# Optimization experiments

Measured on AMD Instinct MI355X. Metric: run time of the kernel, lower is better.

## Reference

```python
import jax, jax.numpy as jnp
import numpy as np
from jax import lax

B, T, CIN, H, W = 2, 6, 1, 256, 256
COUT = 64
L = 13
H2, W2 = H // 2, W // 2


def conv2d(x, w, b, stride=1, pad=0):
    y = lax.conv_general_dilated(x, w, (stride, stride), [(pad, pad), (pad, pad)],
                                 dimension_numbers=('NCHW', 'OIHW', 'NCHW'))
    return y + b[None, :, None, None]


def leaky(x):
    return jnp.where(x >= 0, x, 0.2 * x)


def bilinear_sample(img, sx, sy):
    # img [B,C,H,W]; sx,sy [B,L,H,W] pixel coords; zero padding (grid_sample align_corners=True)
    Bc, C, Hh, Ww = img.shape
    x0 = jnp.floor(sx); y0 = jnp.floor(sy)
    x1 = x0 + 1.0; y1 = y0 + 1.0
    wx1 = sx - x0; wx0 = 1.0 - wx1
    wy1 = sy - y0; wy0 = 1.0 - wy1
    img_flat = img.reshape(Bc, C, Hh * Ww)

    def gather(xi, yi):
        valid = (xi >= 0) & (xi <= Ww - 1) & (yi >= 0) & (yi <= Hh - 1)
        xc = jnp.clip(xi, 0, Ww - 1).astype(jnp.int32)
        yc = jnp.clip(yi, 0, Hh - 1).astype(jnp.int32)
        idx = (yc * Ww + xc).reshape(Bc, 1, -1)
        g = jnp.take_along_axis(img_flat, idx, axis=2).reshape(Bc, C, *xi.shape[1:])
        return g * valid[:, None].astype(img.dtype)  # [B,C,L,H,W]

    return (gather(x0, y0) * (wx0 * wy0)[:, None]
            + gather(x1, y0) * (wx1 * wy0)[:, None]
            + gather(x0, y1) * (wx0 * wy1)[:, None]
            + gather(x1, y1) * (wx1 * wy1)[:, None])


def setup_inputs() -> dict:
    key = jax.random.key(0)
    ks = jax.random.split(key, 14)
    s = 0.05
    return {
        'x': jax.random.normal(ks[0], (B, T, CIN, H, W), jnp.float32),
        'w_stem': jax.random.normal(ks[1], (COUT * T, CIN * T, 3, 3), jnp.float32) * s,
        'b_stem': jnp.zeros((COUT * T,), jnp.float32),
        'w_i2h': jax.random.normal(ks[2], (3 * COUT, COUT, 3, 3), jnp.float32) * s,
        'b_i2h': jnp.zeros((3 * COUT,), jnp.float32),
        'w_i2f': jax.random.normal(ks[3], (32, COUT, 5, 5), jnp.float32) * s,
        'b_i2f': jnp.zeros((32,), jnp.float32),
        'w_h2f': jax.random.normal(ks[4], (32, COUT, 5, 5), jnp.float32) * s,
        'b_h2f': jnp.zeros((32,), jnp.float32),
        'w_flow': jax.random.normal(ks[5], (L * 2, 32, 5, 5), jnp.float32) * s,
        'b_flow': jnp.zeros((L * 2,), jnp.float32),
        'w_ret': jax.random.normal(ks[6], (3 * COUT, L * COUT, 1, 1), jnp.float32) * s,
        'b_ret': jnp.zeros((3 * COUT,), jnp.float32),
    }


def reference(x, w_stem, b_stem, w_i2h, b_i2h, w_i2f, b_i2f, w_h2f, b_h2f,
              w_flow, b_flow, w_ret, b_ret):
    Bq, Tq, Cq, Hq, Wq = x.shape
    h2, w2 = Hq // 2, Wq // 2
    # stem: fold T into channels, strided conv + leaky relu
    xs = x.reshape(Bq, Tq * Cq, Hq, Wq)
    ys = leaky(conv2d(xs, w_stem, b_stem, stride=2, pad=1))
    ys = ys.reshape(Bq, Tq, COUT, h2, w2)
    seq = jnp.transpose(ys, (1, 0, 2, 3, 4))  # [T,B,C,h,w]

    gy, gx = jnp.meshgrid(jnp.arange(h2, dtype=jnp.float32),
                          jnp.arange(w2, dtype=jnp.float32), indexing='ij')

    def step(hprev, xt):
        i2h = conv2d(xt, w_i2h, b_i2h, pad=1)  # [B,3C,h,w]
        f1 = leaky(conv2d(xt, w_i2f, b_i2f, pad=2) + conv2d(hprev, w_h2f, b_h2f, pad=2))
        flows = conv2d(f1, w_flow, b_flow, pad=2).reshape(Bq, L, 2, h2, w2)
        u, v = flows[:, :, 0], flows[:, :, 1]
        # wrap(h, -flow): sample at grid - flow
        sx = gx[None, None] - u
        sy = gy[None, None] - v
        warped = bilinear_sample(hprev, sx, sy)  # [B,C,L,h,w]
        warped = jnp.transpose(warped, (0, 2, 1, 3, 4)).reshape(Bq, L * COUT, h2, w2)
        h2h = conv2d(warped, w_ret, b_ret)  # 1x1 conv
        ir, iu, im = jnp.split(i2h, 3, axis=1)
        hr, hu, hm = jnp.split(h2h, 3, axis=1)
        r = jax.nn.sigmoid(ir + hr)
        z = jax.nn.sigmoid(iu + hu)
        m = leaky(im + r * hm)
        hnext = z * hprev + (1.0 - z) * m
        return hnext, hnext

    h0 = jnp.zeros((Bq, COUT, h2, w2), x.dtype)
    _, outs = lax.scan(step, h0, seq)  # [T,B,C,h,w]
    return jnp.transpose(outs, (1, 0, 2, 3, 4))
```

## Files before the change

kernel.cpp:

```cpp
#include <hip/hip_runtime.h>
#include <cstddef>

#define NPIX 16384
#define T_ 6

typedef __attribute__((ext_vector_type(8))) short bf16x8;
typedef __attribute__((ext_vector_type(4))) short bf16x4;
typedef __attribute__((ext_vector_type(4))) float f32x4;
typedef __attribute__((ext_vector_type(4))) unsigned u32x4;
typedef __attribute__((ext_vector_type(2))) unsigned u32x2;

__device__ __forceinline__ float leakyf(float x){ return x >= 0.f ? x : 0.2f*x; }
__device__ __forceinline__ float sigmf(float x){ return 1.f/(1.f+__expf(-x)); }
__device__ __forceinline__ short f2bf(float f){
    unsigned u = __float_as_uint(f);
    u += 0x7fffu + ((u>>16)&1u);
    return (short)(u>>16);
}
__device__ __forceinline__ float bf2f(short s){
    return __uint_as_float(((unsigned)(unsigned short)s)<<16);
}
__device__ __forceinline__ unsigned cvtpk(float lo, float hi){
    unsigned d;
    asm("v_cvt_pk_bf16_f32 %0, %1, %2" : "=v"(d) : "v"(lo), "v"(hi));
    return d;
}
__device__ __forceinline__ f32x4 MFMA(bf16x8 a, bf16x8 b, f32x4 c){
    return __builtin_amdgcn_mfma_f32_16x16x32_bf16(a, b, c, 0, 0, 0);
}

__global__ __launch_bounds__(256) void prep_w(const float* __restrict__ wi2h,
        const float* __restrict__ wf1i, const float* __restrict__ wf1h,
        const float* __restrict__ wfl, const float* __restrict__ wrt,
        const float* __restrict__ wst, short* __restrict__ dst){
    int idx = blockIdx.x*256 + threadIdx.x;
    float v;
    if(idx < 110592){
        int kk = idx/12288, r = idx%12288, oc = r>>6, ic = r&63;
        v = wi2h[((size_t)(oc*64+ic))*9 + kk];
    } else if(idx < 212992){
        int j = idx-110592; int tap = j>>11, r = j&2047, oc = r>>6, ic = r&63;
        int inp = tap/25, q = tap%25;
        const float* s = inp ? wf1h : wf1i;
        v = s[((size_t)(oc*64+ic))*25 + q];
    } else if(idx < 238592){
        int j = idx-212992; int q = j>>10, r = j&1023, oc = r>>5, ic = r&31;
        v = (oc < 26) ? wfl[((size_t)(oc*32+ic))*25 + q] : 0.f;
    } else if(idx < 398336){
        int j = idx-238592; int s_ = j/6144, r = j%6144, oc = r>>5, c = r&31;
        v = wrt[(size_t)oc*832 + s_*32 + c];
    } else {
        int j = idx-398336; int oc = j>>6, k = j&63;
        if(k < 54){ int ic = k/9, kk = k%9; v = wst[((size_t)(oc*6+ic))*9 + kk]; }
        else v = 0.f;
    }
    dst[idx] = f2bf(v);
}

__global__ __launch_bounds__(256) void stem_mfma(const float* __restrict__ x,
        const short* __restrict__ wS, const float* __restrict__ bias, short* __restrict__ ys_cl){
    __shared__ float xh[6*17*18];
    int bx = blockIdx.x;
    int ohalf = bx & 1, tile = (bx>>1) & 255, b = bx>>9;
    int ty0 = (tile>>4)*8, tx0 = (tile&15)*8;
    int tid = threadIdx.x, wid = tid>>6, lane = tid&63, lr = lane&15, lg = lane>>4;
    int iy0 = ty0*2-1, ix0 = tx0*2-1;
    for(int i=tid; i<1734; i+=256){
        int ic = i/289, r = i%289, hy = r/17, hx = r%17;
        int iy = iy0+hy, ix = ix0+hx;
        float v = 0.f;
        if((unsigned)iy<256u && (unsigned)ix<256u) v = x[((size_t)b*6+ic)*65536 + iy*256 + ix];
        xh[(ic*17+hy)*18+hx] = v;
    }
    __syncthreads();
    int pxl = wid*16 + lr;
    int ry = (pxl>>3)*2, rx = (pxl&7)*2;
    bf16x8 a[2];
    #pragma unroll
    for(int cg=0; cg<2; ++cg){
        #pragma unroll
        for(int e=0; e<8; ++e){
            int k = cg*32 + lg*8 + e;
            float v = 0.f;
            if(k < 54){
                int ic = k/9, t9 = k%9, ky = t9/3, kx = t9%3;
                v = xh[(ic*17 + ry+ky)*18 + rx+kx];
            }
            a[cg][e] = f2bf(v);
        }
    }
    short* yb = ys_cl + (size_t)b*NPIX*384;
    #pragma unroll
    for(int nj=0; nj<12; ++nj){
        int oc = (ohalf*12 + nj)*16 + lr;
        f32x4 acc = {};
        #pragma unroll
        for(int cg=0; cg<2; ++cg){
            bf16x8 bb = *(const bf16x8*)&wS[(size_t)oc*64 + cg*32 + lg*8];
            acc = MFMA(a[cg], bb, acc);
        }
        float bvs = bias[oc];
        #pragma unroll
        for(int r=0; r<4; ++r){
            int pxr = wid*16 + lg*4 + r;
            int pix = (ty0 + (pxr>>3))*128 + tx0 + (pxr&7);
            yb[(size_t)pix*384 + oc] = f2bf(leakyf(acc[r]+bvs));
        }
    }
}

__global__ __launch_bounds__(512) void ih_if_mfma(const short* __restrict__ ys_cl,
        const short* __restrict__ wI, const float* __restrict__ bI,
        const short* __restrict__ wF,
        short* __restrict__ i2h_all, float* __restrict__ f1i_all){
    __shared__ short xt[432*72];
    int bx = blockIdx.x;
    int tile = bx & 63; int r_ = bx >> 6; int t = r_ % 6; int b = r_ / 6;
    int ty0 = (tile>>2)*8, tx0 = (tile&3)*32;
    int tid = threadIdx.x, wid = tid>>6, lane = tid&63, lr = lane&15, lg = lane>>4;
    int mw = wid>>2, nw = wid&3;
    const short* xb = ys_cl + (size_t)b*NPIX*384 + t*64;
    for(int i=tid; i<3456; i+=512){
        int pix = i>>3, c8 = i&7;
        int hy = pix/36, hx = pix - hy*36;
        int py = ty0 - 2 + hy, px = tx0 - 2 + hx;
        bf16x8 v = {};
        if((unsigned)py < 128u && (unsigned)px < 128u)
            v = *(const bf16x8*)&xb[((size_t)py*128 + px)*384 + c8*8];
        *(bf16x8*)&xt[pix*72 + c8*8] = v;
    }
    __syncthreads();
    f32x4 accI[4][2][3] = {};
    for(int kk=0; kk<9; ++kk){
        int ky = kk/3, kx = kk - ky*3;
        #pragma unroll
        for(int cg=0; cg<2; ++cg){
            bf16x8 bv[3];
            #pragma unroll
            for(int ni=0; ni<3; ++ni)
                bv[ni] = *(const bf16x8*)&wI[((size_t)kk*192 + nw*48 + ni*16 + lr)*64 + cg*32 + lg*8];
            #pragma unroll
            for(int ri=0; ri<4; ++ri){
                int r2 = mw*4 + ri;
                bf16x8 av[2];
                #pragma unroll
                for(int mi=0; mi<2; ++mi){
                    int hp = (r2 + ky + 1)*36 + mi*16 + lr + kx + 1;
                    av[mi] = *(const bf16x8*)&xt[hp*72 + cg*32 + lg*8];
                }
                #pragma unroll
                for(int mi=0; mi<2; ++mi)
                  #pragma unroll
                  for(int ni=0; ni<3; ++ni)
                    accI[ri][mi][ni] = MFMA(av[mi], bv[ni], accI[ri][mi][ni]);
            }
        }
    }
    short* oI = i2h_all + ((size_t)t*2 + b)*192*NPIX;
    #pragma unroll
    for(int ri=0; ri<4; ++ri){
        int py = ty0 + mw*4 + ri;
        #pragma unroll
        for(int mi=0; mi<2; ++mi){
            int px = tx0 + mi*16 + lg*4;
            #pragma unroll
            for(int ni=0; ni<3; ++ni){
                int oc = nw*48 + ni*16 + lr;
                float bvs = bI[oc];
                f32x4 r = accI[ri][mi][ni];
                u32x2 st;
                st[0] = cvtpk(r[0]+bvs, r[1]+bvs);
                st[1] = cvtpk(r[2]+bvs, r[3]+bvs);
                *(u32x2*)&oI[(size_t)oc*NPIX + py*128 + px] = st;
            }
        }
    }
    f32x4 accF[4] = {};
    int mif = nw>>1, jF = (nw&1)*16 + lr;
    for(int q=0; q<25; ++q){
        int ky = q/5, kx = q - ky*5;
        #pragma unroll
        for(int cg=0; cg<2; ++cg){
            bf16x8 bb = *(const bf16x8*)&wF[((size_t)q*32 + (nw&1)*16 + lr)*64 + cg*32 + lg*8];
            #pragma unroll
            for(int ri=0; ri<4; ++ri){
                int hp = (mw*4 + ri + ky)*36 + mif*16 + lr + kx;
                bf16x8 av = *(const bf16x8*)&xt[hp*72 + cg*32 + lg*8];
                accF[ri] = MFMA(av, bb, accF[ri]);
            }
        }
    }
    float* oF = f1i_all + ((size_t)t*2 + b)*32*NPIX;
    #pragma unroll
    for(int ri=0; ri<4; ++ri){
        int py = ty0 + mw*4 + ri;
        int px = tx0 + mif*16 + lg*4;
        *(f32x4*)&oF[(size_t)jF*NPIX + py*128 + px] = accF[ri];
    }
}

__global__ __launch_bounds__(256) void f1h_mfma(const short* __restrict__ h_cl,
        const short* __restrict__ wF, const float* __restrict__ f1i_all, int t,
        const float* __restrict__ bi, const float* __restrict__ bh,
        short* __restrict__ f1_cl){
    __shared__ short xt[144*72];
    int bx = blockIdx.x;
    int tile = bx & 255, b = bx>>8;
    int ty0 = (tile>>4)*8, tx0 = (tile&15)*8;
    int tid = threadIdx.x, wid = tid>>6, lane = tid&63, lr = lane&15, lg = lane>>4;
    int mw = wid>>1, nw = wid&1;
    const short* xb = h_cl + (size_t)b*NPIX*64;
    for(int i=tid; i<1152; i+=256){
        int pix = i>>3, c8 = i&7;
        int hy = pix/12, hx = pix - hy*12;
        int py = ty0 - 2 + hy, px = tx0 - 2 + hx;
        bf16x8 v = {};
        if((unsigned)py < 128u && (unsigned)px < 128u)
            v = *(const bf16x8*)&xb[((size_t)py*128 + px)*64 + c8*8];
        *(bf16x8*)&xt[pix*72 + c8*8] = v;
    }
    __syncthreads();
    f32x4 acc[2] = {};
    for(int q=0; q<25; ++q){
        int ky = q/5, kx = q - ky*5;
        #pragma unroll
        for(int cg=0; cg<2; ++cg){
            bf16x8 av[2];
            #pragma unroll
            for(int mi=0; mi<2; ++mi){
                int m = mw*32 + mi*16 + lr;
                int hp = ((m>>3)+ky)*12 + (m&7)+kx;
                av[mi] = *(const bf16x8*)&xt[hp*72 + cg*32 + lg*8];
            }
            bf16x8 bb = *(const bf16x8*)&wF[((size_t)(25+q)*32 + nw*16 + lr)*64 + cg*32 + lg*8];
            #pragma unroll
            for(int mi=0; mi<2; ++mi) acc[mi] = MFMA(av[mi], bb, acc[mi]);
        }
    }
    int j = nw*16 + lr;
    float bvs = bi[j] + bh[j];
    const float* pF = f1i_all + ((size_t)t*2 + b)*32*NPIX;
    __syncthreads();
    #pragma unroll
    for(int mi=0; mi<2; ++mi){
        int m0 = mw*32 + mi*16 + lg*4;
        int py = ty0 + (m0>>3), px = tx0 + (m0&7);
        f32x4 p = *(const f32x4*)&pF[(size_t)j*NPIX + py*128 + px];
        #pragma unroll
        for(int r=0; r<4; ++r) xt[(m0+r)*40 + j] = f2bf(leakyf(acc[mi][r] + p[r] + bvs));
    }
    __syncthreads();
    {
        int px = tid>>2, c8 = tid&3;
        int pix = (ty0 + (px>>3))*128 + tx0 + (px&7);
        *(bf16x8*)&f1_cl[((size_t)b*NPIX + pix)*32 + c8*8] = *(const bf16x8*)&xt[px*40 + c8*8];
    }
}

__global__ __launch_bounds__(256) void flow_mfma(const short* __restrict__ f1_cl,
        const short* __restrict__ wA, const float* __restrict__ bias, float* __restrict__ flows){
    __shared__ short xt[144*40];
    int bx = blockIdx.x;
    int tile = bx & 255, b = bx>>8;
    int ty0 = (tile>>4)*8, tx0 = (tile&15)*8;
    int tid = threadIdx.x, wid = tid>>6, lane = tid&63, lr = lane&15, lg = lane>>4;
    int mw = wid>>1, nw = wid&1;
    f32x4 acc[2] = {};
    const short* xb = f1_cl + (size_t)b*NPIX*32;
    for(int i=tid; i<576; i+=256){
        int pix = i>>2, c8 = i&3;
        int hy = pix/12, hx = pix - hy*12;
        int py = ty0 - 2 + hy, px = tx0 - 2 + hx;
        bf16x8 v = {};
        if((unsigned)py < 128u && (unsigned)px < 128u)
            v = *(const bf16x8*)&xb[((size_t)py*128 + px)*32 + c8*8];
        *(bf16x8*)&xt[pix*40 + c8*8] = v;
    }
    __syncthreads();
    for(int ky=0; ky<5; ++ky){
        #pragma unroll
        for(int kx=0; kx<5; ++kx){
            bf16x8 av[2];
            #pragma unroll
            for(int mi=0; mi<2; ++mi){
                int m = mw*32 + mi*16 + lr;
                int hp = ((m>>3)+ky)*12 + (m&7) + kx;
                av[mi] = *(const bf16x8*)&xt[hp*40 + lg*8];
            }
            bf16x8 bb = *(const bf16x8*)&wA[((size_t)((ky*5+kx)*32) + nw*16 + lr)*32 + lg*8];
            #pragma unroll
            for(int mi=0; mi<2; ++mi) acc[mi] = MFMA(av[mi], bb, acc[mi]);
        }
    }
    int j = nw*16 + lr;
    if(j < 26){
        float bvs = bias[j];
        #pragma unroll
        for(int mi=0; mi<2; ++mi){
            int m0 = mw*32 + mi*16 + lg*4;
            int py = ty0 + (m0>>3), px = tx0 + (m0&7);
            f32x4 r = acc[mi];
            f32x4 st; st[0]=r[0]+bvs; st[1]=r[1]+bvs; st[2]=r[2]+bvs; st[3]=r[3]+bvs;
            *(f32x4*)&flows[((size_t)b*26 + j)*NPIX + py*128 + px] = st;
        }
    }
}

__device__ __forceinline__ void calc_corners(const float* __restrict__ s_sx,
        const float* __restrict__ s_sy, int l, int mypx,
        int& i00, int& i10, int& i01, int& i11,
        float& w00, float& w10, float& w01, float& w11){
    float sx = s_sx[l*64+mypx], sy = s_sy[l*64+mypx];
    float x0f = floorf(sx), y0f = floorf(sy);
    int x0 = (int)x0f, y0 = (int)y0f;
    float wx1 = sx-x0f, wy1 = sy-y0f, wx0 = 1.f-wx1, wy0 = 1.f-wy1;
    bool vx0 = (unsigned)x0<128u, vx1 = (unsigned)(x0+1)<128u;
    bool vy0 = (unsigned)y0<128u, vy1 = (unsigned)(y0+1)<128u;
    w00 = (vx0&&vy0)? wx0*wy0 : 0.f;
    w10 = (vx1&&vy0)? wx1*wy0 : 0.f;
    w01 = (vx0&&vy1)? wx0*wy1 : 0.f;
    w11 = (vx1&&vy1)? wx1*wy1 : 0.f;
    int xc0 = max(0,min(127,x0)), xc1 = max(0,min(127,x0+1));
    int yc0 = max(0,min(127,y0)), yc1 = max(0,min(127,y0+1));
    i00 = yc0*128+xc0; i10 = yc0*128+xc1; i01 = yc1*128+xc0; i11 = yc1*128+xc1;
}

__global__ __launch_bounds__(256) void warpret_mfma(
        const float* __restrict__ hprev_f32, int hstride,
        const short* __restrict__ h_in,
        const float* __restrict__ flows,
        const short* __restrict__ wret, const float* __restrict__ b_ret,
        const short* __restrict__ ib_bf, float* __restrict__ out,
        short* __restrict__ h_out, int t){
    __shared__ float s_sx[832], s_sy[832];
    __shared__ short At[2][64*40];
    __shared__ short Bt[2][192*40];
    int bx = blockIdx.x;
    int half = bx & 1, row = (bx>>1) & 127, b = bx >> 8;
    int pxbase = half*64;
    int tid = threadIdx.x, wid = tid>>6, lane = tid&63, lr = lane&15, lg = lane>>4;
    const short* hc = h_in + (size_t)b*NPIX*64;
    f32x4 acc[12] = {};
    for(int i=tid; i<832; i+=256){
        int l = i>>6, px = i&63;
        float u = flows[((size_t)b*26 + 2*l)*NPIX + row*128 + pxbase + px];
        float v = flows[((size_t)b*26 + 2*l+1)*NPIX + row*128 + pxbase + px];
        s_sx[i] = (float)(pxbase+px) - u;
        s_sy[i] = (float)row - v;
    }
    __syncthreads();

    int spx = tid & 63, sch = tid >> 6;
    int brow = tid >> 2, bc4 = tid & 3;

    auto issue = [&](int sp, bf16x8& g00, bf16x8& g10, bf16x8& g01, bf16x8& g11,
                     bf16x8& q0, bf16x8& q1, bf16x8& q2,
                     float& w00, float& w10, float& w01, float& w11){
        int i00,i10,i01,i11;
        calc_corners(s_sx, s_sy, sp>>1, spx, i00,i10,i01,i11, w00,w10,w01,w11);
        int cb = (sp&1)*32 + sch*8;
        g00 = *(const bf16x8*)&hc[(size_t)i00*64 + cb];
        g10 = *(const bf16x8*)&hc[(size_t)i10*64 + cb];
        g01 = *(const bf16x8*)&hc[(size_t)i01*64 + cb];
        g11 = *(const bf16x8*)&hc[(size_t)i11*64 + cb];
        q0 = *(const bf16x8*)&wret[((size_t)sp*192 + brow      )*32 + bc4*8];
        q1 = *(const bf16x8*)&wret[((size_t)sp*192 + brow +  64)*32 + bc4*8];
        q2 = *(const bf16x8*)&wret[((size_t)sp*192 + brow + 128)*32 + bc4*8];
    };
    auto commit = [&](int buf, bf16x8 g00, bf16x8 g10, bf16x8 g01, bf16x8 g11,
                      bf16x8 q0, bf16x8 q1, bf16x8 q2,
                      float w00, float w10, float w01, float w11){
        float r[8];
        #pragma unroll
        for(int e=0; e<8; ++e)
            r[e] = bf2f(g00[e])*w00 + bf2f(g10[e])*w10 +
                   bf2f(g01[e])*w01 + bf2f(g11[e])*w11;
        u32x4 av;
        av[0] = cvtpk(r[0], r[1]);
        av[1] = cvtpk(r[2], r[3]);
        av[2] = cvtpk(r[4], r[5]);
        av[3] = cvtpk(r[6], r[7]);
        *(u32x4*)&At[buf][spx*40 + sch*8] = av;
        *(bf16x8*)&Bt[buf][(brow      )*40 + bc4*8] = q0;
        *(bf16x8*)&Bt[buf][(brow +  64)*40 + bc4*8] = q1;
        *(bf16x8*)&Bt[buf][(brow + 128)*40 + bc4*8] = q2;
    };

    {
        bf16x8 g00,g10,g01,g11,q0,q1,q2; float w00,w10,w01,w11;
        issue(0, g00,g10,g01,g11,q0,q1,q2, w00,w10,w01,w11);
        commit(0, g00,g10,g01,g11,q0,q1,q2, w00,w10,w01,w11);
    }
    bf16x8 p00,p10,p01,p11,pq0,pq1,pq2; float v00,v10,v01,v11;
    issue(1, p00,p10,p01,p11,pq0,pq1,pq2, v00,v10,v01,v11);
    __syncthreads();

    for(int s=0; s<26; ++s){
        int cur = s & 1, nxt = cur ^ 1;
        bf16x8 n00,n10,n01,n11,nq0,nq1,nq2; float u00,u10,u01,u11;
        if(s < 24)
            issue(s+2, n00,n10,n01,n11,nq0,nq1,nq2, u00,u10,u01,u11);
        {
            bf16x8 a = *(const bf16x8*)&At[cur][(wid*16 + lr)*40 + lg*8];
            #pragma unroll
            for(int ni=0; ni<12; ++ni){
                bf16x8 bb = *(const bf16x8*)&Bt[cur][(ni*16 + lr)*40 + lg*8];
                acc[ni] = MFMA(a, bb, acc[ni]);
            }
        }
        if(s < 25)
            commit(nxt, p00,p10,p01,p11,pq0,pq1,pq2, v00,v10,v01,v11);
        __syncthreads();
        if(s < 24){
            p00=n00; p10=n10; p01=n01; p11=n11;
            pq0=nq0; pq1=nq1; pq2=nq2;
            v00=u00; v10=u10; v01=u01; v11=u11;
        }
    }

    short* Ht = &Bt[0][0];
    const short* ib = ib_bf + (size_t)b*192*NPIX + row*128 + pxbase;
    const float* hbf = hprev_f32 + (size_t)b*hstride + row*128 + pxbase;
    float* ob = out + (((size_t)b*T_ + t)*64)*NPIX + row*128 + pxbase;
    int px4 = wid*16 + lg*4;
    #pragma unroll
    for(int ni=0; ni<4; ++ni){
        int oc = ni*16 + lr;
        bf16x4 irv = *(const bf16x4*)&ib[(size_t)oc*NPIX + px4];
        bf16x4 iuv = *(const bf16x4*)&ib[(size_t)(64+oc)*NPIX + px4];
        bf16x4 imv = *(const bf16x4*)&ib[(size_t)(128+oc)*NPIX + px4];
        f32x4 hp = *(const f32x4*)&hbf[(size_t)oc*NPIX + px4];
        float br = b_ret[oc], bu = b_ret[64+oc], bm = b_ret[128+oc];
        f32x4 st;
        #pragma unroll
        for(int r=0; r<4; ++r){
            float hr = acc[ni][r] + br;
            float hu = acc[ni+4][r] + bu;
            float hm = acc[ni+8][r] + bm;
            float rg = sigmf(bf2f(irv[r]) + hr);
            float zg = sigmf(bf2f(iuv[r]) + hu);
            float mg = leakyf(bf2f(imv[r]) + rg*hm);
            st[r] = zg*hp[r] + (1.f-zg)*mg;
        }
        *(f32x4*)&ob[(size_t)oc*NPIX + px4] = st;
        #pragma unroll
        for(int r=0; r<4; ++r) Ht[(px4+r)*72 + oc] = f2bf(st[r]);
    }
    __syncthreads();
    short* ho = h_out + ((size_t)b*NPIX + row*128 + pxbase)*64;
    for(int i=tid; i<512; i+=256){
        int px = i>>3, c8 = i&7;
        *(bf16x8*)&ho[(size_t)px*64 + c8*8] = *(const bf16x8*)&Ht[px*72 + c8*8];
    }
}

extern "C" void kernel_launch(void* const* d_in, const int* in_sizes, int n_in,
                              void* d_out, int out_size, void* d_ws, size_t ws_size,
                              hipStream_t stream) {
    const float* x      = (const float*)d_in[0];
    const float* w_stem = (const float*)d_in[1];
    const float* b_stem = (const float*)d_in[2];
    const float* w_i2h  = (const float*)d_in[3];
    const float* b_i2h  = (const float*)d_in[4];
    const float* w_i2f  = (const float*)d_in[5];
    const float* b_i2f  = (const float*)d_in[6];
    const float* w_h2f  = (const float*)d_in[7];
    const float* b_h2f  = (const float*)d_in[8];
    const float* w_flow = (const float*)d_in[9];
    const float* b_flow = (const float*)d_in[10];
    const float* w_ret  = (const float*)d_in[11];
    const float* b_ret  = (const float*)d_in[12];
    float* out = (float*)d_out;

    char* w = (char*)d_ws;
    float* h0_f32  = (float*)w;  w += (size_t)2*64*NPIX*4;
    short* i2h_all = (short*)w;  w += (size_t)6*2*192*NPIX*2;
    float* f1i_all = (float*)w;  w += (size_t)6*2*32*NPIX*4;
    float* flows   = (float*)w;  w += (size_t)2*26*NPIX*4;
    short* ys_cl   = (short*)w;  w += (size_t)2*NPIX*384*2;
    short* h_clA   = (short*)w;  w += (size_t)2*NPIX*64*2;
    short* h_clB   = (short*)w;  w += (size_t)2*NPIX*64*2;
    short* f1_cl   = (short*)w;  w += (size_t)2*NPIX*32*2;
    short* wAbase  = (short*)w;
    short* wA_i2h  = wAbase;
    short* wA_f1   = wAbase + 110592;
    short* wA_flow = wAbase + 212992;
    short* wA_ret  = wAbase + 238592;
    short* wA_stem = wAbase + 398336;

    prep_w<<<1652, 256, 0, stream>>>(w_i2h, w_i2f, w_h2f, w_flow, w_ret, w_stem, wAbase);
    hipMemsetAsync(h0_f32, 0, (size_t)2*64*NPIX*4, stream);
    hipMemsetAsync(h_clA, 0, (size_t)2*NPIX*64*2, stream);

    stem_mfma<<<1024, 256, 0, stream>>>(x, wA_stem, b_stem, ys_cl);
    ih_if_mfma<<<768, 512, 0, stream>>>(ys_cl, wA_i2h, b_i2h, wA_f1, i2h_all, f1i_all);

    for (int t = 0; t < T_; ++t) {
        const float* hprev = (t == 0) ? h0_f32 : out + (size_t)(t - 1) * 64 * NPIX;
        int hstride = (t == 0) ? 64 * NPIX : T_ * 64 * NPIX;
        short* h_in  = (t & 1) ? h_clB : h_clA;
        short* h_nxt = (t & 1) ? h_clA : h_clB;
        f1h_mfma<<<512, 256, 0, stream>>>(h_in, wA_f1, f1i_all, t, b_i2f, b_h2f, f1_cl);
        flow_mfma<<<512, 256, 0, stream>>>(f1_cl, wA_flow, b_flow, flows);
        warpret_mfma<<<512, 256, 0, stream>>>(hprev, hstride, h_in, flows,
                                              wA_ret, b_ret,
                                              i2h_all + (size_t)t*2*192*NPIX,
                                              out, h_nxt, t);
    }
}
```

Measured before the change: 493.2 us.

## Split warp-retrieve kernel into 512 threads with specialized gather and weight-load waves

The warp+1x1-conv kernel moves from 256 to 512 threads per block. The first four waves only gather and bilinear-blend the hidden state, and the other four only stage the weight tiles. The MFMA work is split across two output-channel halves, and the partial accumulators are exchanged through shared memory before the GRU gate epilogue. The aim is more waves in flight to hide gather latency and lower per-thread register pressure. In exchange, prefetch depth drops from two stages to one, and the extra shared-memory reduction plus barrier add overhead.

```diff
diff --git a/kernel.cpp b/kernel.cpp
--- a/kernel.cpp
+++ b/kernel.cpp
@@ -325,7 +325,7 @@
     i00 = yc0*128+xc0; i10 = yc0*128+xc1; i01 = yc1*128+xc0; i11 = yc1*128+xc1;
 }
 
-__global__ __launch_bounds__(256) void warpret_mfma(
+__global__ __launch_bounds__(512) void warpret_mfma(
         const float* __restrict__ hprev_f32, int hstride,
         const short* __restrict__ h_in,
         const float* __restrict__ flows,
@@ -339,9 +339,11 @@
     int half = bx & 1, row = (bx>>1) & 127, b = bx >> 8;
     int pxbase = half*64;
     int tid = threadIdx.x, wid = tid>>6, lane = tid&63, lr = lane&15, lg = lane>>4;
+    int pxw = wid & 3, och = wid >> 2;
+    bool stA = tid < 256;
     const short* hc = h_in + (size_t)b*NPIX*64;
-    f32x4 acc[12] = {};
-    for(int i=tid; i<832; i+=256){
+    f32x4 acc[6] = {};
+    for(int i=tid; i<832; i+=512){
         int l = i>>6, px = i&63;
         float u = flows[((size_t)b*26 + 2*l)*NPIX + row*128 + pxbase + px];
         float v = flows[((size_t)b*26 + 2*l+1)*NPIX + row*128 + pxbase + px];
@@ -350,106 +352,112 @@
     }
     __syncthreads();
 
-    int spx = tid & 63, sch = tid >> 6;
-    int brow = tid >> 2, bc4 = tid & 3;
-
-    auto issue = [&](int sp, bf16x8& g00, bf16x8& g10, bf16x8& g01, bf16x8& g11,
-                     bf16x8& q0, bf16x8& q1, bf16x8& q2,
-                     float& w00, float& w10, float& w01, float& w11){
-        int i00,i10,i01,i11;
-        calc_corners(s_sx, s_sy, sp>>1, spx, i00,i10,i01,i11, w00,w10,w01,w11);
-        int cb = (sp&1)*32 + sch*8;
-        g00 = *(const bf16x8*)&hc[(size_t)i00*64 + cb];
-        g10 = *(const bf16x8*)&hc[(size_t)i10*64 + cb];
-        g01 = *(const bf16x8*)&hc[(size_t)i01*64 + cb];
-        g11 = *(const bf16x8*)&hc[(size_t)i11*64 + cb];
-        q0 = *(const bf16x8*)&wret[((size_t)sp*192 + brow      )*32 + bc4*8];
-        q1 = *(const bf16x8*)&wret[((size_t)sp*192 + brow +  64)*32 + bc4*8];
-        q2 = *(const bf16x8*)&wret[((size_t)sp*192 + brow + 128)*32 + bc4*8];
+    int spx = tid & 63, sch = (tid >> 6) & 3;
+    int st = tid & 255;
+    int brow = st >> 2, bc4 = st & 3;
+
+    bf16x8 g00,g10,g01,g11, q0,q1,q2;
+    float w00=0,w10=0,w01=0,w11=0;
+
+    auto issue = [&](int sp){
+        if(stA){
+            int i00,i10,i01,i11;
+            calc_corners(s_sx, s_sy, sp>>1, spx, i00,i10,i01,i11, w00,w10,w01,w11);
+            int cb = (sp&1)*32 + sch*8;
+            g00 = *(const bf16x8*)&hc[(size_t)i00*64 + cb];
+            g10 = *(const bf16x8*)&hc[(size_t)i10*64 + cb];
+            g01 = *(const bf16x8*)&hc[(size_t)i01*64 + cb];
+            g11 = *(const bf16x8*)&hc[(size_t)i11*64 + cb];
+        } else {
+            q0 = *(const bf16x8*)&wret[((size_t)sp*192 + brow      )*32 + bc4*8];
+            q1 = *(const bf16x8*)&wret[((size_t)sp*192 + brow +  64)*32 + bc4*8];
+            q2 = *(const bf16x8*)&wret[((size_t)sp*192 + brow + 128)*32 + bc4*8];
+        }
     };
-    auto commit = [&](int buf, bf16x8 g00, bf16x8 g10, bf16x8 g01, bf16x8 g11,
-                      bf16x8 q0, bf16x8 q1, bf16x8 q2,
-                      float w00, float w10, float w01, float w11){
-        float r[8];
-        #pragma unroll
-        for(int e=0; e<8; ++e)
-            r[e] = bf2f(g00[e])*w00 + bf2f(g10[e])*w10 +
-                   bf2f(g01[e])*w01 + bf2f(g11[e])*w11;
-        u32x4 av;
-        av[0] = cvtpk(r[0], r[1]);
-        av[1] = cvtpk(r[2], r[3]);
-        av[2] = cvtpk(r[4], r[5]);
-        av[3] = cvtpk(r[6], r[7]);
-        *(u32x4*)&At[buf][spx*40 + sch*8] = av;
-        *(bf16x8*)&Bt[buf][(brow      )*40 + bc4*8] = q0;
-        *(bf16x8*)&Bt[buf][(brow +  64)*40 + bc4*8] = q1;
-        *(bf16x8*)&Bt[buf][(brow + 128)*40 + bc4*8] = q2;
+    auto commit = [&](int buf){
+        if(stA){
+            float r[8];
+            #pragma unroll
+            for(int e=0; e<8; ++e)
+                r[e] = bf2f(g00[e])*w00 + bf2f(g10[e])*w10 +
+                       bf2f(g01[e])*w01 + bf2f(g11[e])*w11;
+            u32x4 av;
+            av[0] = cvtpk(r[0], r[1]);
+            av[1] = cvtpk(r[2], r[3]);
+            av[2] = cvtpk(r[4], r[5]);
+            av[3] = cvtpk(r[6], r[7]);
+            *(u32x4*)&At[buf][spx*40 + sch*8] = av;
+        } else {
+            *(bf16x8*)&Bt[buf][(brow      )*40 + bc4*8] = q0;
+            *(bf16x8*)&Bt[buf][(brow +  64)*40 + bc4*8] = q1;
+            *(bf16x8*)&Bt[buf][(brow + 128)*40 + bc4*8] = q2;
+        }
     };
 
-    {
-        bf16x8 g00,g10,g01,g11,q0,q1,q2; float w00,w10,w01,w11;
-        issue(0, g00,g10,g01,g11,q0,q1,q2, w00,w10,w01,w11);
-        commit(0, g00,g10,g01,g11,q0,q1,q2, w00,w10,w01,w11);
-    }
-    bf16x8 p00,p10,p01,p11,pq0,pq1,pq2; float v00,v10,v01,v11;
-    issue(1, p00,p10,p01,p11,pq0,pq1,pq2, v00,v10,v01,v11);
+    issue(0); commit(0);
     __syncthreads();
 
     for(int s=0; s<26; ++s){
         int cur = s & 1, nxt = cur ^ 1;
-        bf16x8 n00,n10,n01,n11,nq0,nq1,nq2; float u00,u10,u01,u11;
-        if(s < 24)
-            issue(s+2, n00,n10,n01,n11,nq0,nq1,nq2, u00,u10,u01,u11);
+        if(s < 25) issue(s+1);
         {
-            bf16x8 a = *(const bf16x8*)&At[cur][(wid*16 + lr)*40 + lg*8];
-            #pragma unroll
-            for(int ni=0; ni<12; ++ni){
-                bf16x8 bb = *(const bf16x8*)&Bt[cur][(ni*16 + lr)*40 + lg*8];
+            bf16x8 a = *(const bf16x8*)&At[cur][(pxw*16 + lr)*40 + lg*8];
+            #pragma unroll
+            for(int ni=0; ni<6; ++ni){
+                bf16x8 bb = *(const bf16x8*)&Bt[cur][(och*96 + ni*16 + lr)*40 + lg*8];
                 acc[ni] = MFMA(a, bb, acc[ni]);
             }
         }
-        if(s < 25)
-            commit(nxt, p00,p10,p01,p11,pq0,pq1,pq2, v00,v10,v01,v11);
+        if(s < 25) commit(nxt);
         __syncthreads();
-        if(s < 24){
-            p00=n00; p10=n10; p01=n01; p11=n11;
-            pq0=nq0; pq1=nq1; pq2=nq2;
-            v00=u00; v10=u10; v01=u01; v11=u11;
-        }
-    }
-
-    short* Ht = &Bt[0][0];
-    const short* ib = ib_bf + (size_t)b*192*NPIX + row*128 + pxbase;
-    const float* hbf = hprev_f32 + (size_t)b*hstride + row*128 + pxbase;
-    float* ob = out + (((size_t)b*T_ + t)*64)*NPIX + row*128 + pxbase;
-    int px4 = wid*16 + lg*4;
-    #pragma unroll
-    for(int ni=0; ni<4; ++ni){
-        int oc = ni*16 + lr;
-        bf16x4 irv = *(const bf16x4*)&ib[(size_t)oc*NPIX + px4];
-        bf16x4 iuv = *(const bf16x4*)&ib[(size_t)(64+oc)*NPIX + px4];
-        bf16x4 imv = *(const bf16x4*)&ib[(size_t)(128+oc)*NPIX + px4];
-        f32x4 hp = *(const f32x4*)&hbf[(size_t)oc*NPIX + px4];
-        float br = b_ret[oc], bu = b_ret[64+oc], bm = b_ret[128+oc];
-        f32x4 st;
-        #pragma unroll
-        for(int r=0; r<4; ++r){
-            float hr = acc[ni][r] + br;
-            float hu = acc[ni+4][r] + bu;
-            float hm = acc[ni+8][r] + bm;
-            float rg = sigmf(bf2f(irv[r]) + hr);
-            float zg = sigmf(bf2f(iuv[r]) + hu);
-            float mg = leakyf(bf2f(imv[r]) + rg*hm);
-            st[r] = zg*hp[r] + (1.f-zg)*mg;
-        }
-        *(f32x4*)&ob[(size_t)oc*NPIX + px4] = st;
-        #pragma unroll
-        for(int r=0; r<4; ++r) Ht[(px4+r)*72 + oc] = f2bf(st[r]);
-    }
-    __syncthreads();
-    short* ho = h_out + ((size_t)b*NPIX + row*128 + pxbase)*64;
-    for(int i=tid; i<512; i+=256){
-        int px = i>>3, c8 = i&7;
+    }
+
+    float* redf = (float*)&Bt[0][0];
+    short* Ht   = &At[0][0];
+    int px4 = pxw*16 + lg*4;
+    if(och == 1){
+        #pragma unroll
+        for(int ni=0; ni<6; ++ni)
+          #pragma unroll
+          for(int r=0; r<4; ++r)
+            redf[(px4+r)*96 + ni*16 + lr] = acc[ni][r];
+    }
+    __syncthreads();
+    if(och == 0){
+        const short* ib = ib_bf + (size_t)b*192*NPIX + row*128 + pxbase;
+        const float* hbf = hprev_f32 + (size_t)b*hstride + row*128 + pxbase;
+        float* ob = out + (((size_t)b*T_ + t)*64)*NPIX + row*128 + pxbase;
+        #pragma unroll
+        for(int ni=0; ni<4; ++ni){
+            int oc = ni*16 + lr;
+            bf16x4 irv = *(const bf16x4*)&ib[(size_t)oc*NPIX + px4];
+            bf16x4 iuv = *(const bf16x4*)&ib[(size_t)(64+oc)*NPIX + px4];
+            bf16x4 imv = *(const bf16x4*)&ib[(size_t)(128+oc)*NPIX + px4];
+            f32x4 hp = *(const f32x4*)&hbf[(size_t)oc*NPIX + px4];
+            float br = b_ret[oc], bu = b_ret[64+oc], bm = b_ret[128+oc];
+            f32x4 stv;
+            #pragma unroll
+            for(int r=0; r<4; ++r){
+                float hr = acc[ni][r] + br;
+                float hu_raw = (ni < 2) ? acc[4+ni][r]
+                               : redf[(px4+r)*96 + (ni-2)*16 + lr];
+                float hm_raw = redf[(px4+r)*96 + 32 + ni*16 + lr];
+                float hu = hu_raw + bu;
+                float hm = hm_raw + bm;
+                float rg = sigmf(bf2f(irv[r]) + hr);
+                float zg = sigmf(bf2f(iuv[r]) + hu);
+                float mg = leakyf(bf2f(imv[r]) + rg*hm);
+                stv[r] = zg*hp[r] + (1.f-zg)*mg;
+            }
+            *(f32x4*)&ob[(size_t)oc*NPIX + px4] = stv;
+            #pragma unroll
+            for(int r=0; r<4; ++r) Ht[(px4+r)*72 + oc] = f2bf(stv[r]);
+        }
+    }
+    __syncthreads();
+    {
+        int px = tid>>3, c8 = tid&7;
+        short* ho = h_out + ((size_t)b*NPIX + row*128 + pxbase)*64;
         *(bf16x8*)&ho[(size_t)px*64 + c8*8] = *(const bf16x8*)&Ht[px*72 + c8*8];
     }
 }
@@ -502,7 +510,7 @@
         short* h_nxt = (t & 1) ? h_clA : h_clB;
         f1h_mfma<<<512, 256, 0, stream>>>(h_in, wA_f1, f1i_all, t, b_i2f, b_h2f, f1_cl);
         flow_mfma<<<512, 256, 0, stream>>>(f1_cl, wA_flow, b_flow, flows);
-        warpret_mfma<<<512, 256, 0, stream>>>(hprev, hstride, h_in, flows,
+        warpret_mfma<<<512, 512, 0, stream>>>(hprev, hstride, h_in, flows,
                                               wA_ret, b_ret,
                                               i2h_all + (size_t)t*2*192*NPIX,
                                               out, h_nxt, t);
```

Result: slower. 588.0 us (+19.2%).
